# Optimization experiments

Hardware: AMD Instinct MI355X
Metric: run time of the kernel (lower is better)

## Reference

```python
import jax, jax.numpy as jnp
import numpy as np

B, H, W = 8, 640, 640
THRESH = 0.6       # self.threshold in Pnet_post
NMS_IOU = 0.3      # iou threshold passed in post_data_Pnet
MAX_DET = 128      # fixed detection budget (padded greedy NMS)


def _tffix(x):
    # tf fix(): floor toward zero
    return jnp.where(x >= 0, jnp.floor(x), jnp.ceil(x))


def _rec2square(rect):
    # rect: [N,5] (x1,y1,x2,y2,score) -> squared boxes
    x1, y1, x2, y2, s = rect[:, 0], rect[:, 1], rect[:, 2], rect[:, 3], rect[:, 4]
    w = x2 - x1
    h = y2 - y1
    l = jnp.maximum(w, h)
    nx1 = x1 + w * 0.5 - l * 0.5
    ny1 = y1 + h * 0.5 - l * 0.5
    return jnp.stack([nx1, ny1, nx1 + l, ny1 + l, s], axis=1)


def _greedy_nms(rect, valid):
    # rect: [N,5]; valid: [N] bool (score >= THRESH). Sequential greedy NMS
    # (highest score first, suppress iou > NMS_IOU), padded to MAX_DET rows.
    x1, y1, x2, y2 = rect[:, 0], rect[:, 1], rect[:, 2], rect[:, 3]
    area = (x2 - x1 + 1.0) * (y2 - y1 + 1.0)
    s0 = jnp.where(valid, rect[:, 4], -jnp.inf)

    def step(s, _):
        i = jnp.argmax(s)
        alive = jnp.isfinite(s[i])
        xx1 = jnp.maximum(x1[i], x1)
        yy1 = jnp.maximum(y1[i], y1)
        xx2 = jnp.minimum(x2[i], x2)
        yy2 = jnp.minimum(y2[i], y2)
        inter = jnp.maximum(0.0, xx2 - xx1 + 1.0) * jnp.maximum(0.0, yy2 - yy1 + 1.0)
        iou = inter / (area[i] + area - inter)
        s_next = jnp.where(iou > NMS_IOU, -jnp.inf, s).at[i].set(-jnp.inf)
        s_next = jnp.where(alive, s_next, s)
        return s_next, (i, alive)

    _, (picks, alive) = jax.lax.scan(step, s0, None, length=MAX_DET)
    out = rect[picks]                       # [MAX_DET,5]
    return jnp.where(alive[:, None], out, 0.0)


def _post_single(cls, roi, scale, h_raw, w_raw):
    # cls: [H,W,2], roi: [H,W,4], scale/h_raw/w_raw: scalars
    h, w = cls.shape[0], cls.shape[1]
    score = cls[:, :, 1].T                  # [W,H] == Cls_pro[...,0]
    offset = jnp.transpose(roi, (1, 0, 2))  # [W,H,4] == stacked dx1..dx4
    out_side = max(w, h)
    stride = 0.0 if out_side == 1 else (2.0 * out_side + 11.0 - 12.0) / (out_side - 1.0)
    sc = 1.0 / scale                        # scale arg of _cls_bb2rect is 1/scale
    ii = jnp.broadcast_to(jnp.arange(w, dtype=jnp.float32)[:, None], (w, h))
    jj = jnp.broadcast_to(jnp.arange(h, dtype=jnp.float32)[None, :], (w, h))
    idx = jnp.stack([ii, jj], axis=-1)      # [W,H,2] grid coords (thresh_index)
    bb1 = _tffix(stride * idx * sc)
    bb2 = _tffix((stride * idx + 11.0) * sc)
    box = jnp.concatenate([bb1, bb2], axis=-1) + offset * 12.0 * sc  # [W,H,4]
    rect = jnp.concatenate([box, score[..., None]], axis=-1).reshape(-1, 5)
    rect = _rec2square(rect)
    # pick_rect: clip to image, swap inverted corners
    x1 = jnp.maximum(0.0, rect[:, 0])
    y1 = jnp.maximum(0.0, rect[:, 1])
    x2 = jnp.minimum(w_raw, rect[:, 2])
    y2 = jnp.minimum(h_raw, rect[:, 3])
    inv = (x1 > x2) | (y1 > y2)
    fx1 = jnp.where(inv, jnp.minimum(x1, x2), x1)
    fy1 = jnp.where(inv, jnp.minimum(y1, y2), y1)
    fx2 = jnp.where(inv, jnp.maximum(x1, x2), x2)
    fy2 = jnp.where(inv, jnp.maximum(y1, y2), y2)
    pick = jnp.stack([fx1, fy1, fx2, fy2, rect[:, 4]], axis=1)
    valid = score.reshape(-1) >= THRESH     # dynamic threshold -> mask
    return _greedy_nms(pick, valid)


def setup_inputs() -> dict:
    key = jax.random.key(0)
    k1, k2, k3 = jax.random.split(key, 3)
    classifier = jax.random.uniform(k1, (B, H, W, 2), dtype=jnp.float32)
    bbox_regress = jax.random.normal(k2, (B, H, W, 4), dtype=jnp.float32) * 0.1
    scale = jax.random.uniform(k3, (B,), dtype=jnp.float32, minval=0.4, maxval=1.0)
    height_raw = jnp.full((B, 1), 1500.0, dtype=jnp.float32)
    width_raw = jnp.full((B, 1), 1500.0, dtype=jnp.float32)
    return {"classifier": classifier, "bbox_regress": bbox_regress,
            "scale": scale, "height_raw": height_raw, "width_raw": width_raw}


def reference(classifier, bbox_regress, scale, height_raw, width_raw):
    # -> [B, MAX_DET, 5]; rows beyond #detections are zero
    return jax.vmap(_post_single)(classifier, bbox_regress, scale,
                                  height_raw[:, 0], width_raw[:, 0])
```

## Files before the change

kernel.cpp:

```cpp
#include <hip/hip_runtime.h>

#define Bn 8
#define Hn 640
#define Wn 640
#define CELLS (Hn*Wn)
#define NBIN 1024
#define HB 16
#define CB 32
#define CAP 4096
#define KTGT 3584u
#define MAXD 128
#define STAGE 512

#define WS_PART_BYTE 64
#define WS_KEYS_BYTE (64 + Bn*HB*NBIN*2)

__global__ void k_hist(const float4* __restrict__ cls4, unsigned short* __restrict__ part) {
    __shared__ unsigned h[NBIN];
    int b = blockIdx.y, blk = blockIdx.x, tid = threadIdx.x;
    for (int p = tid; p < NBIN; p += 256) h[p] = 0u;
    __syncthreads();
    const float4* src = cls4 + ((size_t)b * CELLS + blk * (CELLS / HB)) / 2;
    for (int k = 0; k < (CELLS / HB / 2) / 256; ++k) {
        float4 v = src[k * 256 + tid];
        if (v.y >= 0.6f) {
            int bin = min((int)((v.y - 0.6f) * 2560.0f), NBIN - 1);
            atomicAdd(&h[bin], 1u);
        }
        if (v.w >= 0.6f) {
            int bin = min((int)((v.w - 0.6f) * 2560.0f), NBIN - 1);
            atomicAdd(&h[bin], 1u);
        }
    }
    __syncthreads();
    unsigned short* dst = part + (size_t)(b * HB + blk) * NBIN;
    for (int p = tid; p < NBIN; p += 256) dst[p] = (unsigned short)h[p];
}

__global__ void k_cut(const unsigned short* __restrict__ part, float* __restrict__ cut,
                      unsigned* __restrict__ cnt) {
    __shared__ unsigned h[NBIN];
    __shared__ int best;
    int b = blockIdx.x, tid = threadIdx.x;
    unsigned acc[NBIN / 256];
    for (int q = 0; q < NBIN / 256; ++q) acc[q] = 0u;
    for (int blk = 0; blk < HB; ++blk) {
        const unsigned short* src = part + (size_t)(b * HB + blk) * NBIN;
        for (int q = 0; q < NBIN / 256; ++q) acc[q] += src[q * 256 + tid];
    }
    for (int q = 0; q < NBIN / 256; ++q) h[q * 256 + tid] = acc[q];
    if (tid == 0) { best = 0; cnt[b] = 0u; }
    __syncthreads();
    for (int off = 1; off < NBIN; off <<= 1) {
        unsigned v[NBIN / 256];
        for (int q = 0; q < NBIN / 256; ++q) {
            int p = q * 256 + tid;
            v[q] = h[p] + ((p + off < NBIN) ? h[p + off] : 0u);
        }
        __syncthreads();
        for (int q = 0; q < NBIN / 256; ++q) h[q * 256 + tid] = v[q];
        __syncthreads();
    }
    for (int q = 0; q < NBIN / 256; ++q) {
        int p = q * 256 + tid;
        if (h[p] >= KTGT && (p == NBIN - 1 || h[p + 1] < KTGT)) best = p;
    }
    __syncthreads();
    if (tid == 0) cut[b] = 0.6f + (float)best * (0.4f / (float)NBIN);
}

__global__ void k_compact(const float4* __restrict__ cls4, const float* __restrict__ cut,
                          unsigned* __restrict__ cnt, unsigned long long* __restrict__ keys) {
    __shared__ unsigned long long buf[STAGE];
    __shared__ unsigned lcnt, gbase;
    int b = blockIdx.y, blk = blockIdx.x, tid = threadIdx.x;
    float c = cut[b];
    if (tid == 0) lcnt = 0u;
    __syncthreads();
    int cellbase = blk * (CELLS / CB);
    const float4* src = cls4 + ((size_t)b * CELLS + cellbase) / 2;
    for (int k = 0; k < (CELLS / CB / 2) / 256; ++k) {
        float4 v = src[k * 256 + tid];
        int mm = cellbase + (k * 256 + tid) * 2;
        #pragma unroll
        for (int c2 = 0; c2 < 2; ++c2) {
            float s = c2 ? v.w : v.y;
            if (s >= c) {
                unsigned idx = atomicAdd(&lcnt, 1u);
                if (idx < STAGE) {
                    int m2 = mm + c2;
                    int i = m2 % Wn, j = m2 / Wn;
                    unsigned n = (unsigned)(i * Hn + j);
                    buf[idx] = ((unsigned long long)__float_as_uint(s) << 32) |
                               (unsigned long long)(~n);
                }
            }
        }
    }
    __syncthreads();
    unsigned total = min(lcnt, (unsigned)STAGE);
    if (tid == 0) gbase = atomicAdd(&cnt[b], total);
    __syncthreads();
    unsigned gb = gbase;
    for (unsigned i = tid; i < total; i += 256) {
        unsigned slot = gb + i;
        if (slot < CAP) keys[(size_t)b * CAP + slot] = buf[i];
    }
}

__device__ __forceinline__ void make_box(int n, float sc, float WR, float HR,
                                         const float4* __restrict__ roi4b,
                                         float& fx1, float& fy1, float& fx2, float& fy2,
                                         float& area) {
    const float stride = (float)(1279.0 / 639.0);
    int i = n / Hn, j = n % Hn;
    float fi = (float)i, fj = (float)j;
    float b1x = truncf((stride * fi) * sc);
    float b1y = truncf((stride * fj) * sc);
    float b2x = truncf((stride * fi + 11.0f) * sc);
    float b2y = truncf((stride * fj + 11.0f) * sc);
    float4 off = roi4b[j * Wn + i];
    float x1 = b1x + (off.x * 12.0f) * sc;
    float y1 = b1y + (off.y * 12.0f) * sc;
    float x2 = b2x + (off.z * 12.0f) * sc;
    float y2 = b2y + (off.w * 12.0f) * sc;
    float w = x2 - x1, h = y2 - y1;
    float l = fmaxf(w, h);
    float nx1 = x1 + w * 0.5f - l * 0.5f;
    float ny1 = y1 + h * 0.5f - l * 0.5f;
    float nx2 = nx1 + l, ny2 = ny1 + l;
    float cx1 = fmaxf(0.0f, nx1), cy1 = fmaxf(0.0f, ny1);
    float cx2 = fminf(WR, nx2),   cy2 = fminf(HR, ny2);
    bool inv = (cx1 > cx2) || (cy1 > cy2);
    fx1 = inv ? fminf(cx1, cx2) : cx1;
    fy1 = inv ? fminf(cy1, cy2) : cy1;
    fx2 = inv ? fmaxf(cx1, cx2) : cx2;
    fy2 = inv ? fmaxf(cy1, cy2) : cy2;
    area = (fx2 - fx1 + 1.0f) * (fy2 - fy1 + 1.0f);
}

__launch_bounds__(1024)
__global__ void k_nms(const float4* __restrict__ roi4, const float* __restrict__ scale,
                      const float* __restrict__ hraw, const float* __restrict__ wraw,
                      const unsigned* __restrict__ cnt,
                      const unsigned long long* __restrict__ keys_g,
                      float* __restrict__ out) {
    __shared__ unsigned long long ks[CAP];
    __shared__ float4 abox[MAXD];
    __shared__ float aarea[MAXD], ascore[MAXD];
    int b = blockIdx.x, tid = threadIdx.x;
    int mn = (int)min(cnt[b], (unsigned)CAP);
    for (int p = tid; p < CAP; p += 1024)
        ks[p] = (p < mn) ? keys_g[(size_t)b * CAP + p] : 0ULL;
    __syncthreads();
    for (int k = 2; k <= CAP; k <<= 1) {
        for (int j = k >> 1; j > 0; j >>= 1) {
            for (int p = tid; p < CAP; p += 1024) {
                int ixj = p ^ j;
                if (ixj > p) {
                    unsigned long long a = ks[p], c = ks[ixj];
                    bool descBlk = ((p & k) == 0);
                    if (descBlk ? (a < c) : (a > c)) { ks[p] = c; ks[ixj] = a; }
                }
            }
            __syncthreads();
        }
    }
    if (tid < 64) {
        int lane = tid;
        float sc = 1.0f / scale[b];
        float WR = wraw[b], HR = hraw[b];
        const float4* roi4b = roi4 + (size_t)b * CELLS;
        int n_acc = 0, pos = 0;
        while (pos < mn && n_acc < MAXD) {
            int myp = pos + lane;
            bool has = myp < mn;
            unsigned long long key = has ? ks[myp] : 0ULL;
            float s = __uint_as_float((unsigned)(key >> 32));
            unsigned n = ~(unsigned)key;
            float fx1, fy1, fx2, fy2, area;
            make_box(has ? (int)n : 0, sc, WR, HR, roi4b, fx1, fy1, fx2, fy2, area);
            bool rejected = !has;
            for (int k2 = 0; k2 < n_acc; ++k2) {
                float4 bb = abox[k2];
                float va = aarea[k2];
                float iw = fminf(fx2, bb.z) - fmaxf(fx1, bb.x) + 1.0f;
                float ih = fminf(fy2, bb.w) - fmaxf(fy1, bb.y) + 1.0f;
                float inter = fmaxf(0.0f, iw) * fmaxf(0.0f, ih);
                float iou = inter / (area + va - inter);
                rejected |= (iou > 0.3f);
            }
            unsigned long long active = __ballot(!rejected);
            while (active && n_acc < MAXD) {
                int f = __ffsll(active) - 1;
                float bx1 = __shfl(fx1, f), by1 = __shfl(fy1, f);
                float bx2 = __shfl(fx2, f), by2 = __shfl(fy2, f);
                float bar = __shfl(area, f), bs = __shfl(s, f);
                if (lane == 0) {
                    abox[n_acc] = make_float4(bx1, by1, bx2, by2);
                    aarea[n_acc] = bar;
                    ascore[n_acc] = bs;
                }
                if (lane == f) rejected = true;
                if (!rejected) {
                    float iw = fminf(fx2, bx2) - fmaxf(fx1, bx1) + 1.0f;
                    float ih = fminf(fy2, by2) - fmaxf(fy1, by1) + 1.0f;
                    float inter = fmaxf(0.0f, iw) * fmaxf(0.0f, ih);
                    float iou = inter / (area + bar - inter);
                    rejected |= (iou > 0.3f);
                }
                n_acc++;
                active = __ballot(!rejected);
            }
            pos += 64;
        }
        for (int q = lane; q < MAXD * 5; q += 64) {
            int k2 = q / 5, c = q % 5;
            float v = 0.0f;
            if (k2 < n_acc) {
                float4 bb = abox[k2];
                v = (c == 0) ? bb.x : (c == 1) ? bb.y : (c == 2) ? bb.z
                    : (c == 3) ? bb.w : ascore[k2];
            }
            out[(b * MAXD + k2) * 5 + c] = v;
        }
    }
}

extern "C" void kernel_launch(void* const* d_in, const int* in_sizes, int n_in,
                              void* d_out, int out_size, void* d_ws, size_t ws_size,
                              hipStream_t stream) {
    const float4* cls4 = (const float4*)d_in[0];
    const float4* roi4 = (const float4*)d_in[1];
    const float* scale = (const float*)d_in[2];
    const float* hraw  = (const float*)d_in[3];
    const float* wraw  = (const float*)d_in[4];
    float* out = (float*)d_out;

    unsigned* cnt = (unsigned*)d_ws;
    float*    cut = (float*)((char*)d_ws + 32);
    unsigned short* part = (unsigned short*)((char*)d_ws + WS_PART_BYTE);
    unsigned long long* keys = (unsigned long long*)((char*)d_ws + WS_KEYS_BYTE);

    hipLaunchKernelGGL(k_hist, dim3(HB, Bn), dim3(256), 0, stream, cls4, part);
    hipLaunchKernelGGL(k_cut, dim3(Bn), dim3(256), 0, stream, part, cut, cnt);
    hipLaunchKernelGGL(k_compact, dim3(CB, Bn), dim3(256), 0, stream, cls4, cut, cnt, keys);
    hipLaunchKernelGGL(k_nms, dim3(Bn), dim3(1024), 0, stream,
                       roi4, scale, hraw, wraw, cnt, keys, out);
}
```

Baseline: 252.1 us.

## Replace bitonic sort plus wave NMS with block-wide argmax greedy NMS

The NMS kernel no longer bitonic-sorts up to 4096 keys in shared memory. Each of the 1024 threads now holds four candidate keys and their precomputed boxes in registers, and every step runs a block-wide argmax (wave shuffle reduction, then a 16-entry shared scan with double-buffered slots), accepts the winner and suppresses overlapping candidates in parallel. This removes the many synchronised sort passes and the serial single-wave acceptance loop, at the cost of one __syncthreads per accepted detection, up to 128 of them. The histogram is also doubled to 2048 bins for a finer threshold cut, which makes the partial-histogram and scan work larger.

```diff
diff --git a/kernel.cpp b/kernel.cpp
--- a/kernel.cpp
+++ b/kernel.cpp
@@ -4,16 +4,18 @@
 #define Hn 640
 #define Wn 640
 #define CELLS (Hn*Wn)
-#define NBIN 1024
+#define NBIN 2048
 #define HB 16
 #define CB 32
 #define CAP 4096
 #define KTGT 3584u
 #define MAXD 128
 #define STAGE 512
-
-#define WS_PART_BYTE 64
-#define WS_KEYS_BYTE (64 + Bn*HB*NBIN*2)
+#define RSLOT 4
+
+#define WS_CUT_BYTE 256
+#define WS_PART_BYTE 512
+#define WS_KEYS_BYTE (512 + Bn*HB*NBIN*2)
 
 __global__ void k_hist(const float4* __restrict__ cls4, unsigned short* __restrict__ part) {
     __shared__ unsigned h[NBIN];
@@ -24,11 +26,11 @@
     for (int k = 0; k < (CELLS / HB / 2) / 256; ++k) {
         float4 v = src[k * 256 + tid];
         if (v.y >= 0.6f) {
-            int bin = min((int)((v.y - 0.6f) * 2560.0f), NBIN - 1);
+            int bin = min((int)((v.y - 0.6f) * 5120.0f), NBIN - 1);
             atomicAdd(&h[bin], 1u);
         }
         if (v.w >= 0.6f) {
-            int bin = min((int)((v.w - 0.6f) * 2560.0f), NBIN - 1);
+            int bin = min((int)((v.w - 0.6f) * 5120.0f), NBIN - 1);
             atomicAdd(&h[bin], 1u);
         }
     }
@@ -37,44 +39,45 @@
     for (int p = tid; p < NBIN; p += 256) dst[p] = (unsigned short)h[p];
 }
 
-__global__ void k_cut(const unsigned short* __restrict__ part, float* __restrict__ cut,
+__global__ void k_cut(const unsigned short* __restrict__ part, float* __restrict__ cutv,
                       unsigned* __restrict__ cnt) {
     __shared__ unsigned h[NBIN];
     __shared__ int best;
     int b = blockIdx.x, tid = threadIdx.x;
-    unsigned acc[NBIN / 256];
-    for (int q = 0; q < NBIN / 256; ++q) acc[q] = 0u;
+    const int Q = NBIN / 256;
+    unsigned acc[Q];
+    for (int q = 0; q < Q; ++q) acc[q] = 0u;
     for (int blk = 0; blk < HB; ++blk) {
         const unsigned short* src = part + (size_t)(b * HB + blk) * NBIN;
-        for (int q = 0; q < NBIN / 256; ++q) acc[q] += src[q * 256 + tid];
-    }
-    for (int q = 0; q < NBIN / 256; ++q) h[q * 256 + tid] = acc[q];
+        for (int q = 0; q < Q; ++q) acc[q] += src[q * 256 + tid];
+    }
+    for (int q = 0; q < Q; ++q) h[q * 256 + tid] = acc[q];
     if (tid == 0) { best = 0; cnt[b] = 0u; }
     __syncthreads();
     for (int off = 1; off < NBIN; off <<= 1) {
-        unsigned v[NBIN / 256];
-        for (int q = 0; q < NBIN / 256; ++q) {
+        unsigned v[Q];
+        for (int q = 0; q < Q; ++q) {
             int p = q * 256 + tid;
             v[q] = h[p] + ((p + off < NBIN) ? h[p + off] : 0u);
         }
         __syncthreads();
-        for (int q = 0; q < NBIN / 256; ++q) h[q * 256 + tid] = v[q];
+        for (int q = 0; q < Q; ++q) h[q * 256 + tid] = v[q];
         __syncthreads();
     }
-    for (int q = 0; q < NBIN / 256; ++q) {
+    for (int q = 0; q < Q; ++q) {
         int p = q * 256 + tid;
         if (h[p] >= KTGT && (p == NBIN - 1 || h[p + 1] < KTGT)) best = p;
     }
     __syncthreads();
-    if (tid == 0) cut[b] = 0.6f + (float)best * (0.4f / (float)NBIN);
-}
-
-__global__ void k_compact(const float4* __restrict__ cls4, const float* __restrict__ cut,
+    if (tid == 0) cutv[b] = 0.6f + (float)best * (0.4f / (float)NBIN);
+}
+
+__global__ void k_compact(const float4* __restrict__ cls4, const float* __restrict__ cutv,
                           unsigned* __restrict__ cnt, unsigned long long* __restrict__ keys) {
     __shared__ unsigned long long buf[STAGE];
     __shared__ unsigned lcnt, gbase;
     int b = blockIdx.y, blk = blockIdx.x, tid = threadIdx.x;
-    float c = cut[b];
+    float c = cutv[b];
     if (tid == 0) lcnt = 0u;
     __syncthreads();
     int cellbase = blk * (CELLS / CB);
@@ -83,12 +86,12 @@
         float4 v = src[k * 256 + tid];
         int mm = cellbase + (k * 256 + tid) * 2;
         #pragma unroll
-        for (int c2 = 0; c2 < 2; ++c2) {
-            float s = c2 ? v.w : v.y;
+        for (int half = 0; half < 2; ++half) {
+            float s = half ? v.w : v.y;
             if (s >= c) {
                 unsigned idx = atomicAdd(&lcnt, 1u);
                 if (idx < STAGE) {
-                    int m2 = mm + c2;
+                    int m2 = mm + half;
                     int i = m2 % Wn, j = m2 / Wn;
                     unsigned n = (unsigned)(i * Hn + j);
                     buf[idx] = ((unsigned long long)__float_as_uint(s) << 32) |
@@ -110,8 +113,7 @@
 
 __device__ __forceinline__ void make_box(int n, float sc, float WR, float HR,
                                          const float4* __restrict__ roi4b,
-                                         float& fx1, float& fy1, float& fx2, float& fy2,
-                                         float& area) {
+                                         float& fx1, float& fy1, float& fx2, float& fy2) {
     const float stride = (float)(1279.0 / 639.0);
     int i = n / Hn, j = n % Hn;
     float fi = (float)i, fj = (float)j;
@@ -136,7 +138,6 @@
     fy1 = inv ? fminf(cy1, cy2) : cy1;
     fx2 = inv ? fmaxf(cx1, cx2) : cx2;
     fy2 = inv ? fmaxf(cy1, cy2) : cy2;
-    area = (fx2 - fx1 + 1.0f) * (fy2 - fy1 + 1.0f);
 }
 
 __launch_bounds__(1024)
@@ -145,79 +146,101 @@
                       const unsigned* __restrict__ cnt,
                       const unsigned long long* __restrict__ keys_g,
                       float* __restrict__ out) {
-    __shared__ unsigned long long ks[CAP];
+    __shared__ unsigned long long wkey[2][16];
+    __shared__ float4 wbox[2][16];
+    __shared__ float warea[2][16];
     __shared__ float4 abox[MAXD];
-    __shared__ float aarea[MAXD], ascore[MAXD];
+    __shared__ float ascore[MAXD];
     int b = blockIdx.x, tid = threadIdx.x;
+    int wave = tid >> 6, lane = tid & 63;
     int mn = (int)min(cnt[b], (unsigned)CAP);
-    for (int p = tid; p < CAP; p += 1024)
-        ks[p] = (p < mn) ? keys_g[(size_t)b * CAP + p] : 0ULL;
-    __syncthreads();
-    for (int k = 2; k <= CAP; k <<= 1) {
-        for (int j = k >> 1; j > 0; j >>= 1) {
-            for (int p = tid; p < CAP; p += 1024) {
-                int ixj = p ^ j;
-                if (ixj > p) {
-                    unsigned long long a = ks[p], c = ks[ixj];
-                    bool descBlk = ((p & k) == 0);
-                    if (descBlk ? (a < c) : (a > c)) { ks[p] = c; ks[ixj] = a; }
+
+    float sc = 1.0f / scale[b];
+    float WR = wraw[b], HR = hraw[b];
+    const float4* roi4b = roi4 + (size_t)b * CELLS;
+
+    unsigned long long k_[RSLOT];
+    float4 bx_[RSLOT];
+    float ar_[RSLOT];
+    #pragma unroll
+    for (int r = 0; r < RSLOT; ++r) {
+        int idx = r * 1024 + tid;
+        k_[r] = (idx < mn) ? keys_g[(size_t)b * CAP + idx] : 0ULL;
+        bx_[r] = make_float4(0.f, 0.f, 0.f, 0.f);
+        ar_[r] = 1.0f;
+        if (k_[r]) {
+            unsigned n = ~(unsigned)k_[r];
+            float fx1, fy1, fx2, fy2;
+            make_box((int)n, sc, WR, HR, roi4b, fx1, fy1, fx2, fy2);
+            bx_[r] = make_float4(fx1, fy1, fx2, fy2);
+            ar_[r] = (fx2 - fx1 + 1.0f) * (fy2 - fy1 + 1.0f);
+        }
+    }
+
+    int nacc = 0;
+    int p = 0;
+    while (true) {
+        unsigned long long m = k_[0];
+        #pragma unroll
+        for (int r = 1; r < RSLOT; ++r) m = (k_[r] > m) ? k_[r] : m;
+        #pragma unroll
+        for (int off = 1; off < 64; off <<= 1) {
+            unsigned long long o = __shfl_xor(m, off);
+            m = (o > m) ? o : m;
+        }
+        bool mine = false;
+        float4 selb = make_float4(0.f, 0.f, 0.f, 0.f);
+        float sela = 1.0f;
+        #pragma unroll
+        for (int r = 0; r < RSLOT; ++r) {
+            if (m != 0ULL && k_[r] == m) { mine = true; selb = bx_[r]; sela = ar_[r]; }
+        }
+        unsigned long long bal = __ballot(mine);
+        int flead = (int)(__ffsll((long long)bal) - 1);
+        if (m != 0ULL && lane == flead) {
+            wkey[p][wave] = m; wbox[p][wave] = selb; warea[p][wave] = sela;
+        }
+        if (m == 0ULL && lane == 0) wkey[p][wave] = 0ULL;
+        __syncthreads();
+        unsigned long long best = 0ULL;
+        int bw = 0;
+        #pragma unroll
+        for (int w = 0; w < 16; ++w) {
+            unsigned long long v = wkey[p][w];
+            if (v > best) { best = v; bw = w; }
+        }
+        if (best == 0ULL) break;
+        float4 B = wbox[p][bw];
+        float BA = warea[p][bw];
+        if (tid == 0) {
+            abox[nacc] = B;
+            ascore[nacc] = __uint_as_float((unsigned)(best >> 32));
+        }
+        nacc++;
+        if (nacc >= MAXD) break;
+        #pragma unroll
+        for (int r = 0; r < RSLOT; ++r) {
+            if (k_[r]) {
+                if (k_[r] == best) {
+                    k_[r] = 0ULL;
+                } else {
+                    float iw = fminf(bx_[r].z, B.z) - fmaxf(bx_[r].x, B.x) + 1.0f;
+                    float ih = fminf(bx_[r].w, B.w) - fmaxf(bx_[r].y, B.y) + 1.0f;
+                    float inter = fmaxf(0.0f, iw) * fmaxf(0.0f, ih);
+                    float iou = inter / (ar_[r] + BA - inter);
+                    if (iou > 0.3f) k_[r] = 0ULL;
                 }
             }
-            __syncthreads();
-        }
-    }
+        }
+        p ^= 1;
+    }
+    __syncthreads();
+
     if (tid < 64) {
-        int lane = tid;
-        float sc = 1.0f / scale[b];
-        float WR = wraw[b], HR = hraw[b];
-        const float4* roi4b = roi4 + (size_t)b * CELLS;
-        int n_acc = 0, pos = 0;
-        while (pos < mn && n_acc < MAXD) {
-            int myp = pos + lane;
-            bool has = myp < mn;
-            unsigned long long key = has ? ks[myp] : 0ULL;
-            float s = __uint_as_float((unsigned)(key >> 32));
-            unsigned n = ~(unsigned)key;
-            float fx1, fy1, fx2, fy2, area;
-            make_box(has ? (int)n : 0, sc, WR, HR, roi4b, fx1, fy1, fx2, fy2, area);
-            bool rejected = !has;
-            for (int k2 = 0; k2 < n_acc; ++k2) {
-                float4 bb = abox[k2];
-                float va = aarea[k2];
-                float iw = fminf(fx2, bb.z) - fmaxf(fx1, bb.x) + 1.0f;
-                float ih = fminf(fy2, bb.w) - fmaxf(fy1, bb.y) + 1.0f;
-                float inter = fmaxf(0.0f, iw) * fmaxf(0.0f, ih);
-                float iou = inter / (area + va - inter);
-                rejected |= (iou > 0.3f);
-            }
-            unsigned long long active = __ballot(!rejected);
-            while (active && n_acc < MAXD) {
-                int f = __ffsll(active) - 1;
-                float bx1 = __shfl(fx1, f), by1 = __shfl(fy1, f);
-                float bx2 = __shfl(fx2, f), by2 = __shfl(fy2, f);
-                float bar = __shfl(area, f), bs = __shfl(s, f);
-                if (lane == 0) {
-                    abox[n_acc] = make_float4(bx1, by1, bx2, by2);
-                    aarea[n_acc] = bar;
-                    ascore[n_acc] = bs;
-                }
-                if (lane == f) rejected = true;
-                if (!rejected) {
-                    float iw = fminf(fx2, bx2) - fmaxf(fx1, bx1) + 1.0f;
-                    float ih = fminf(fy2, by2) - fmaxf(fy1, by1) + 1.0f;
-                    float inter = fmaxf(0.0f, iw) * fmaxf(0.0f, ih);
-                    float iou = inter / (area + bar - inter);
-                    rejected |= (iou > 0.3f);
-                }
-                n_acc++;
-                active = __ballot(!rejected);
-            }
-            pos += 64;
-        }
         for (int q = lane; q < MAXD * 5; q += 64) {
             int k2 = q / 5, c = q % 5;
             float v = 0.0f;
-            if (k2 < n_acc) {
+            if (k2 < nacc) {
                 float4 bb = abox[k2];
                 v = (c == 0) ? bb.x : (c == 1) ? bb.y : (c == 2) ? bb.z
                     : (c == 3) ? bb.w : ascore[k2];
@@ -238,13 +261,13 @@
     float* out = (float*)d_out;
 
     unsigned* cnt = (unsigned*)d_ws;
-    float*    cut = (float*)((char*)d_ws + 32);
+    float*    cutv = (float*)((char*)d_ws + WS_CUT_BYTE);
     unsigned short* part = (unsigned short*)((char*)d_ws + WS_PART_BYTE);
     unsigned long long* keys = (unsigned long long*)((char*)d_ws + WS_KEYS_BYTE);
 
     hipLaunchKernelGGL(k_hist, dim3(HB, Bn), dim3(256), 0, stream, cls4, part);
-    hipLaunchKernelGGL(k_cut, dim3(Bn), dim3(256), 0, stream, part, cut, cnt);
-    hipLaunchKernelGGL(k_compact, dim3(CB, Bn), dim3(256), 0, stream, cls4, cut, cnt, keys);
+    hipLaunchKernelGGL(k_cut, dim3(Bn), dim3(256), 0, stream, part, cutv, cnt);
+    hipLaunchKernelGGL(k_compact, dim3(CB, Bn), dim3(256), 0, stream, cls4, cutv, cnt, keys);
     hipLaunchKernelGGL(k_nms, dim3(Bn), dim3(1024), 0, stream,
                        roi4, scale, hraw, wraw, cnt, keys, out);
 }
```

Result: slower. 536.5 us (+112.9%).
